# Kernel tuning notes

Hardware: AMD Instinct MI355X
Metric: run time of the kernel (lower is better)

Reference implementation:

```python
import jax, jax.numpy as jnp
import numpy as np

N_NODES = 50000
N_EDGES = 800000
D_IN = 128
D_HID = 128
GN_EPS = 1e-5
L2_EPS = 1e-12


def _gcn_conv(x, edge_index, W, b, num_nodes):
    """PyG GCNConv: symmetric normalization with self-loops; x [N, Fin]."""
    src, dst = edge_index[0], edge_index[1]
    loops = jnp.arange(num_nodes, dtype=src.dtype)
    src = jnp.concatenate([src, loops])
    dst = jnp.concatenate([dst, loops])
    ew = jnp.ones(src.shape[0], dtype=x.dtype)
    deg = jax.ops.segment_sum(ew, dst, num_segments=num_nodes)
    dinv = jnp.where(deg > 0, jax.lax.rsqrt(deg), 0.0)
    norm = dinv[src] * dinv[dst]                       # [E+N]
    xw = x @ W                                         # [N, Fout]
    msg = xw[src] * norm[:, None]                      # gather + scale
    out = jax.ops.segment_sum(msg, dst, num_segments=num_nodes)
    return out + b


def _message_norm(x, msg, scale):
    """PyG MessageNorm(learn_scale=True): x + scale * ||x|| * msg/||msg||."""
    msg_n = msg / jnp.maximum(jnp.linalg.norm(msg, axis=-1, keepdims=True), L2_EPS)
    x_norm = jnp.linalg.norm(x, axis=-1, keepdims=True)
    return x + scale * x_norm * msg_n


def _graph_norm(x, weight, bias, mean_scale):
    """PyG GraphNorm, single graph (batch all zeros)."""
    mean = jnp.mean(x, axis=0, keepdims=True)
    out = x - mean * mean_scale
    var = jnp.mean(out * out, axis=0, keepdims=True)
    return weight * out * jax.lax.rsqrt(var + GN_EPS) + bias


def _gelu(x):
    return jax.nn.gelu(x, approximate=False)


def setup_inputs() -> dict:
    key = jax.random.key(0)
    ks = jax.random.split(key, 4)
    X = jax.random.normal(ks[0], (D_IN, N_NODES), dtype=jnp.float32)
    edge_index = jax.random.randint(ks[1], (2, N_EDGES), 0, N_NODES, dtype=jnp.int64)
    W1 = jax.random.normal(ks[2], (D_IN, D_HID), dtype=jnp.float32) * (1.0 / np.sqrt(D_IN))
    b1 = jnp.zeros((D_HID,), dtype=jnp.float32)
    scale1 = jnp.ones((1,), dtype=jnp.float32)
    W2 = jax.random.normal(ks[3], (D_HID, D_IN), dtype=jnp.float32) * (1.0 / np.sqrt(D_HID))
    b2 = jnp.zeros((D_IN,), dtype=jnp.float32)
    scale2 = jnp.ones((1,), dtype=jnp.float32)
    gn_weight = jnp.ones((D_IN,), dtype=jnp.float32)
    gn_bias = jnp.zeros((D_IN,), dtype=jnp.float32)
    gn_mean_scale = jnp.ones((D_IN,), dtype=jnp.float32)
    return {"X": X, "edge_index": edge_index, "W1": W1, "b1": b1, "scale1": scale1,
            "W2": W2, "b2": b2, "scale2": scale2, "gn_weight": gn_weight,
            "gn_bias": gn_bias, "gn_mean_scale": gn_mean_scale}


def reference(X, edge_index, W1, b1, scale1, W2, b2, scale2,
              gn_weight, gn_bias, gn_mean_scale):
    x = X.T                                            # [N, D_IN]
    n = x.shape[0]
    # GCNChain 1
    f = _gelu(_message_norm(x, _gcn_conv(x, edge_index, W1, b1, n), scale1))
    # GCNChain 2
    f = _gelu(_message_norm(f, _gcn_conv(f, edge_index, W2, b2, n), scale2))
    # residual + GraphNorm + GELU
    return _gelu(_graph_norm(f + x, gn_weight, gn_bias, gn_mean_scale))
```

## Files before the change

kernel.cpp:

```cpp
#include <hip/hip_runtime.h>
#include <math.h>

#define D 128
#define CAP 64
#define NBUCK 98
#define BSZ   512
#define CAPB  10240
#define FSPLIT 4
#define FB (BSZ/FSPLIT)

typedef _Float16 h8 __attribute__((ext_vector_type(8)));
typedef float f4x __attribute__((ext_vector_type(4)));

__device__ __forceinline__ float gelu_f(float v){
    return 0.5f * v * (1.0f + erff(v * 0.70710678f));
}

__device__ __forceinline__ void unpack8(uint4 I, int* s){
    s[0] = (int)(I.x & 0xFFFFu); s[1] = (int)(I.x >> 16);
    s[2] = (int)(I.y & 0xFFFFu); s[3] = (int)(I.y >> 16);
    s[4] = (int)(I.z & 0xFFFFu); s[5] = (int)(I.z >> 16);
    s[6] = (int)(I.w & 0xFFFFu); s[7] = (int)(I.w >> 16);
}

__device__ __forceinline__ h8 gather_accum(const h8* __restrict__ y,
                                           const unsigned short* __restrict__ sp,
                                           int m, int lane, h8 a0){
    h8 z = {0,0,0,0,0,0,0,0};
    h8 a1 = z, a2 = z, a3 = z;
    int j = 0;
    for (; j + 16 <= m; j += 16){
        const uint4* spv = (const uint4*)(sp + j);
        uint4 I0 = spv[0], I1 = spv[1];
        int s[16];
        unpack8(I0, s); unpack8(I1, s + 8);
        h8 v[16];
        #pragma unroll
        for (int i = 0; i < 16; i++) v[i] = y[(size_t)s[i]*16 + lane];
        #pragma unroll
        for (int i = 0; i < 16; i += 4){
            a0 += v[i]; a1 += v[i+1]; a2 += v[i+2]; a3 += v[i+3];
        }
    }
    for (; j + 8 <= m; j += 8){
        const uint4* spv = (const uint4*)(sp + j);
        uint4 I0 = spv[0];
        int s[8];
        unpack8(I0, s);
        h8 v[8];
        #pragma unroll
        for (int i = 0; i < 8; i++) v[i] = y[(size_t)s[i]*16 + lane];
        #pragma unroll
        for (int i = 0; i < 8; i += 4){
            a0 += v[i]; a1 += v[i+1]; a2 += v[i+2]; a3 += v[i+3];
        }
    }
    for (; j + 4 <= m; j += 4){
        const uint2* spv = (const uint2*)(sp + j);
        uint2 I = spv[0];
        int s0 = (int)(I.x & 0xFFFFu), s1 = (int)(I.x >> 16);
        int s2 = (int)(I.y & 0xFFFFu), s3 = (int)(I.y >> 16);
        h8 v0 = y[(size_t)s0*16 + lane];
        h8 v1 = y[(size_t)s1*16 + lane];
        h8 v2 = y[(size_t)s2*16 + lane];
        h8 v3 = y[(size_t)s3*16 + lane];
        a0 += v0; a1 += v1; a2 += v2; a3 += v3;
    }
    for (; j < m; j++) a1 += y[(size_t)sp[j]*16 + lane];
    return (a0 + a1) + (a2 + a3);
}

__global__ void k_init(float* colsum, float* colsq, int* gcur,
                       const float* __restrict__ W1, const float* __restrict__ W2,
                       _Float16* __restrict__ wz1, _Float16* __restrict__ wz2){
    int i = blockIdx.x*blockDim.x + threadIdx.x;
    if (i < D){ colsum[i] = 0.f; colsq[i] = 0.f; }
    if (i < NBUCK) gcur[i] = 0;
    if (i < 32768){
        const float* W = (i < 16384) ? W1 : W2;
        _Float16* wz   = (i < 16384) ? wz1 : wz2;
        int u = i & 16383;
        int jj = u & 7, l = (u>>3)&63, fi = u>>9;
        int kb = fi>>3, j = fi&7;
        int k = kb*32 + (l>>4)*8 + jj;
        int c = j*16 + (l&15);
        wz[u] = (_Float16)W[k*D + c];
    }
}

__global__ __launch_bounds__(256)
void k_part(const int* __restrict__ ei, int* __restrict__ gcur,
            unsigned int* __restrict__ ebin, int E){
    __shared__ int bcnt[NBUCK], bbase[NBUCK], bcur[NBUCK];
    int t = threadIdx.x;
    int chunk = (E + gridDim.x - 1) / gridDim.x;
    int e0 = blockIdx.x*chunk, e1 = min(e0 + chunk, E);
    if (t < NBUCK){ bcnt[t] = 0; bcur[t] = 0; }
    __syncthreads();
    int sl[13], dl[13];
    #pragma unroll
    for (int k = 0; k < 13; k++){
        int e = e0 + t + k*256;
        sl[k] = -1;
        if (e < e1){
            sl[k] = __builtin_nontemporal_load(&ei[e]);
            dl[k] = __builtin_nontemporal_load(&ei[E + e]);
            atomicAdd(&bcnt[dl[k] >> 9], 1);
        }
    }
    __syncthreads();
    if (t < NBUCK) bbase[t] = atomicAdd(&gcur[t], bcnt[t]);
    __syncthreads();
    #pragma unroll
    for (int k = 0; k < 13; k++){
        if (sl[k] >= 0){
            int d = dl[k], b = d >> 9;
            int p = atomicAdd(&bcur[b], 1);
            int idx = bbase[b] + p;
            if (idx < CAPB)
                ebin[(size_t)b*CAPB + idx] = ((unsigned)(d & (BSZ-1)) << 16) | (unsigned)sl[k];
        }
    }
}

__global__ __launch_bounds__(256)
void k_fill2(const unsigned int* __restrict__ ebin, const int* __restrict__ gcur,
             int* __restrict__ cnt, unsigned short* __restrict__ csrc, int N){
    __shared__ unsigned short slab[FB*CAP];
    __shared__ int lcnt[FB];
    int bb = blockIdx.x, b = bb >> 2, part = bb & 3;
    int t = threadIdx.x;
    for (int i = t; i < FB; i += 256) lcnt[i] = 0;
    __syncthreads();
    int cntb = gcur[b]; if (cntb > CAPB) cntb = CAPB;
    const unsigned int* bp = ebin + (size_t)b*CAPB;
    for (int e = t; e < cntb; e += 256){
        unsigned pk = __builtin_nontemporal_load(&bp[e]);
        int dl = pk >> 16;
        if ((dl >> 7) == part){
            int dsub = dl & (FB-1);
            int p = atomicAdd(&lcnt[dsub], 1);
            if (p < CAP) slab[dsub*CAP + p] = (unsigned short)(pk & 0xFFFF);
        }
    }
    __syncthreads();
    int base = b*BSZ + part*FB;
    int nvalid = N - base; if (nvalid > FB) nvalid = FB; if (nvalid < 0) nvalid = 0;
    uint4* dst = (uint4*)&csrc[(size_t)base*CAP];
    const uint4* src = (const uint4*)slab;
    for (int i = t; i < nvalid*8; i += 256) dst[i] = src[i];
    for (int i = t; i < nvalid; i += 256) cnt[base + i] = lcnt[i];
}

__launch_bounds__(256)
__global__ void k_gemm_mfma(const float* __restrict__ in, const h8* __restrict__ wz,
                            const int* __restrict__ cnt, _Float16* __restrict__ outh,
                            h8* __restrict__ xt16, int N){
    __shared__ _Float16 a_lds[8192];
    int t = threadIdx.x;
    int n0 = blockIdx.x * 64;

    #pragma unroll
    for (int i = 0; i < 32; i++){
        int idx = i*256 + t;
        int k = idx >> 6, nn = idx & 63;
        int n = n0 + nn;
        float v = (n < N) ? in[(size_t)k*N + n] : 0.f;
        int kb = k>>5, ks = k&31;
        int lane = (ks>>3)*16 + (nn&15);
        int w = nn>>4;
        a_lds[((kb*4 + w)*64 + lane)*8 + (ks&7)] = (_Float16)v;
    }
    __syncthreads();

    int w = t>>6, l = t&63;
    f4x acc[8];
    #pragma unroll
    for (int j = 0; j < 8; j++) acc[j] = (f4x){0.f, 0.f, 0.f, 0.f};
    #pragma unroll
    for (int kb = 0; kb < 4; kb++){
        h8 a = *(const h8*)&a_lds[((kb*4 + w)*64 + l)*8];
        #pragma unroll
        for (int j = 0; j < 8; j++){
            h8 b = wz[(kb*8 + j)*64 + l];
            acc[j] = __builtin_amdgcn_mfma_f32_16x16x32_f16(a, b, acc[j], 0, 0, 0);
        }
    }

    int quad = l>>4, m = l&15;
    #pragma unroll
    for (int r = 0; r < 4; r++){
        int node = n0 + w*16 + quad*4 + r;
        if (node < N){
            float dv = rsqrtf((float)(cnt[node] + 1));
            #pragma unroll
            for (int j = 0; j < 8; j++)
                outh[(size_t)node*D + j*16 + m] = (_Float16)(acc[j][r] * dv);
        }
    }

    {
        int node = t>>2, kb = t&3;
        int n = n0 + node;
        if (n < N){
            #pragma unroll
            for (int q = 0; q < 4; q++){
                h8 v = *(const h8*)&a_lds[((kb*4 + (node>>4))*64 + q*16 + (node&15))*8];
                xt16[(size_t)n*16 + kb*4 + q] = v;
            }
        }
    }
}

__launch_bounds__(256, 4)
__global__ void k_gath1(const h8* __restrict__ y, const h8* __restrict__ resid,
                        const int* __restrict__ cnt,
                        const unsigned short* __restrict__ csrc,
                        const float* __restrict__ bias, const float* __restrict__ scale,
                        const h8* __restrict__ wz,
                        h8* __restrict__ f1out, _Float16* __restrict__ y2out, int N){
    __shared__ _Float16 a_lds[16*17*8];
    int t = threadIdx.x;
    int n0 = blockIdx.x * 16;
    int g = t >> 4, lane = t & 15;
    int n = n0 + g;
    bool valid = (n < N);

    h8 a0 = {0,0,0,0,0,0,0,0};
    int m = 0; float dv = 1.f;
    if (valid){
        int mraw = cnt[n];
        dv = rsqrtf((float)(mraw + 1));
        m = (mraw < CAP) ? mraw : CAP;
        a0 = y[(size_t)n*16 + lane];
    }
    const unsigned short* sp = csrc + (size_t)n*CAP;
    h8 ah = gather_accum(y, sp, m, lane, a0);

    const float4* bp = (const float4*)&bias[lane*8];
    float4 b0 = bp[0], b1v = bp[1];
    float c[8], r[8];
    float nc = 0.f, nr = 0.f;
    h8 rv = {0,0,0,0,0,0,0,0};
    if (valid) rv = resid[(size_t)n*16 + lane];
    #pragma unroll
    for (int i = 0; i < 8; i++){
        float bb = (i < 4) ? (&b0.x)[i] : (&b1v.x)[i-4];
        c[i] = bb + dv * (float)ah[i];
        nc += c[i]*c[i];
        r[i] = (float)rv[i];
        nr += r[i]*r[i];
    }
    #pragma unroll
    for (int mm = 8; mm > 0; mm >>= 1){
        nc += __shfl_xor(nc, mm, 64);
        nr += __shfl_xor(nr, mm, 64);
    }
    float scl = scale[0] * sqrtf(nr) / fmaxf(sqrtf(nc), 1e-12f);
    h8 o = {0,0,0,0,0,0,0,0};
    if (valid){
        #pragma unroll
        for (int i = 0; i < 8; i++) o[i] = (_Float16)gelu_f(r[i] + scl*c[i]);
        f1out[(size_t)n*16 + lane] = o;
    }
    *(h8*)&a_lds[(g*17 + lane)*8] = o;
    __syncthreads();

    int w = t >> 6, l = t & 63;
    f4x acc0 = {0.f,0.f,0.f,0.f}, acc1 = acc0;
    #pragma unroll
    for (int kb = 0; kb < 4; kb++){
        h8 a = *(const h8*)&a_lds[((l&15)*17 + kb*4 + (l>>4))*8];
        h8 bb0 = wz[(kb*8 + w*2+0)*64 + l];
        h8 bb1 = wz[(kb*8 + w*2+1)*64 + l];
        acc0 = __builtin_amdgcn_mfma_f32_16x16x32_f16(a, bb0, acc0, 0, 0, 0);
        acc1 = __builtin_amdgcn_mfma_f32_16x16x32_f16(a, bb1, acc1, 0, 0, 0);
    }
    int quad = l >> 4, mc = l & 15;
    #pragma unroll
    for (int r2 = 0; r2 < 4; r2++){
        int node = n0 + quad*4 + r2;
        if (node < N){
            float dvn = rsqrtf((float)(cnt[node] + 1));
            y2out[(size_t)node*D + (w*2+0)*16 + mc] = (_Float16)(acc0[r2] * dvn);
            y2out[(size_t)node*D + (w*2+1)*16 + mc] = (_Float16)(acc1[r2] * dvn);
        }
    }
}

__launch_bounds__(256, 4)
__global__ void k_gather2(const h8* __restrict__ y, const h8* __restrict__ resid,
                          const h8* __restrict__ xorig,
                          const int* __restrict__ cnt,
                          const unsigned short* __restrict__ csrc,
                          const float* __restrict__ bias, const float* __restrict__ scale,
                          h8* __restrict__ out16, int N){
    int n = blockIdx.x*16 + (threadIdx.x >> 4);
    if (n >= N) return;
    int lane = threadIdx.x & 15;
    h8 a0 = y[(size_t)n*16 + lane];
    int mraw = cnt[n];
    float dv = rsqrtf((float)(mraw + 1));
    int m = (mraw < CAP) ? mraw : CAP;
    const unsigned short* sp = csrc + (size_t)n*CAP;
    h8 ah = gather_accum(y, sp, m, lane, a0);

    const float4* bp = (const float4*)&bias[lane*8];
    float4 b0 = bp[0], b1v = bp[1];
    float c[8], r[8];
    float nc = 0.f, nr = 0.f;
    h8 rv = resid[(size_t)n*16 + lane];
    #pragma unroll
    for (int i = 0; i < 8; i++){
        float bb = (i < 4) ? (&b0.x)[i] : (&b1v.x)[i-4];
        c[i] = bb + dv * (float)ah[i];
        nc += c[i]*c[i];
        r[i] = (float)rv[i];
        nr += r[i]*r[i];
    }
    #pragma unroll
    for (int mm = 8; mm > 0; mm >>= 1){
        nc += __shfl_xor(nc, mm, 64);
        nr += __shfl_xor(nr, mm, 64);
    }
    float scl = scale[0] * sqrtf(nr) / fmaxf(sqrtf(nc), 1e-12f);
    h8 xv = xorig[(size_t)n*16 + lane];
    h8 o;
    #pragma unroll
    for (int i = 0; i < 8; i++)
        o[i] = (_Float16)(gelu_f(r[i] + scl*c[i]) + (float)xv[i]);
    out16[(size_t)n*16 + lane] = o;
}

__global__ void k_stats(const _Float16* __restrict__ h, float* colsum, float* colsq, int N){
    __shared__ float ls[256], ls2[256];
    int t = threadIdx.x;
    int f = t & 127, half = t >> 7;
    float s = 0.f, s2 = 0.f;
    for (int n = blockIdx.x*2 + half; n < N; n += gridDim.x*2){
        float v = (float)h[(size_t)n*D + f]; s += v; s2 += v*v;
    }
    ls[t] = s; ls2[t] = s2;
    __syncthreads();
    if (t < 128){
        s  = ls[t]  + ls[t+128];
        s2 = ls2[t] + ls2[t+128];
        atomicAdd(&colsum[f], s);
        atomicAdd(&colsq[f], s2);
    }
}

__global__ void k_final(const h8* __restrict__ h16,
                        const float* __restrict__ colsum, const float* __restrict__ colsq,
                        const float* __restrict__ gw, const float* __restrict__ gb,
                        const float* __restrict__ ms,
                        float* __restrict__ outp, int N){
    __shared__ float cf[D], sh[D];
    int t = threadIdx.x;
    if (t < D){
        float invN = 1.0f / (float)N;
        float mean = colsum[t] * invN;
        float c = mean * ms[t];
        float var = colsq[t]*invN - 2.f*c*mean + c*c;
        float a = gw[t] * rsqrtf(var + 1e-5f);
        cf[t] = a;
        sh[t] = gb[t] - c*a;
    }
    __syncthreads();
    int i = blockIdx.x*blockDim.x + t;
    if (i < N*16){
        int n = i >> 4, lane = i & 15;
        h8 v = h16[i];
        int f = lane*8;
        float4 o0, o1;
        o0.x = gelu_f((float)v[0]*cf[f+0] + sh[f+0]);
        o0.y = gelu_f((float)v[1]*cf[f+1] + sh[f+1]);
        o0.z = gelu_f((float)v[2]*cf[f+2] + sh[f+2]);
        o0.w = gelu_f((float)v[3]*cf[f+3] + sh[f+3]);
        o1.x = gelu_f((float)v[4]*cf[f+4] + sh[f+4]);
        o1.y = gelu_f((float)v[5]*cf[f+5] + sh[f+5]);
        o1.z = gelu_f((float)v[6]*cf[f+6] + sh[f+6]);
        o1.w = gelu_f((float)v[7]*cf[f+7] + sh[f+7]);
        *(float4*)&outp[(size_t)n*D + f]     = o0;
        *(float4*)&outp[(size_t)n*D + f + 4] = o1;
    }
}

extern "C" void kernel_launch(void* const* d_in, const int* in_sizes, int n_in,
                              void* d_out, int out_size, void* d_ws, size_t ws_size,
                              hipStream_t stream){
    const float* X   = (const float*)d_in[0];
    const int*   ei  = (const int*)  d_in[1];
    const float* W1  = (const float*)d_in[2];
    const float* b1  = (const float*)d_in[3];
    const float* s1  = (const float*)d_in[4];
    const float* W2  = (const float*)d_in[5];
    const float* b2  = (const float*)d_in[6];
    const float* s2  = (const float*)d_in[7];
    const float* gw  = (const float*)d_in[8];
    const float* gb  = (const float*)d_in[9];
    const float* gms = (const float*)d_in[10];
    int N = in_sizes[0] / D;
    int E = in_sizes[1] / 2;
    float* out = (float*)d_out;

    char* ws = (char*)d_ws;
    size_t o = 0;
    auto alloc = [&](size_t bytes)->void*{
        o = (o + 255) & ~(size_t)255;
        void* p = ws + o; o += bytes; return p;
    };
    int*            cnt    = (int*)           alloc((size_t)N * sizeof(int));
    unsigned short* csrc   = (unsigned short*)alloc((size_t)N * CAP * sizeof(unsigned short));
    unsigned int*   ebin   = (unsigned int*)  alloc((size_t)NBUCK * CAPB * sizeof(unsigned int));
    int*            gcur   = (int*)           alloc(NBUCK * sizeof(int));
    float*          colsum = (float*)         alloc(D * sizeof(float));
    float*          colsq  = (float*)         alloc(D * sizeof(float));
    _Float16*       wz1    = (_Float16*)      alloc(16384 * sizeof(_Float16));
    _Float16*       wz2    = (_Float16*)      alloc(16384 * sizeof(_Float16));
    _Float16*       A      = (_Float16*)      alloc((size_t)N * D * sizeof(_Float16));
    _Float16*       A2     = (_Float16*)      alloc((size_t)N * D * sizeof(_Float16));
    h8*             XT16   = (h8*)            alloc((size_t)N * D * sizeof(_Float16));
    h8*             F1     = (h8*)            alloc((size_t)N * D * sizeof(_Float16));
    h8*             B16    = (h8*)            alloc((size_t)N * D * sizeof(_Float16));

    k_init<<<128, 256, 0, stream>>>(colsum, colsq, gcur, W1, W2, wz1, wz2);
    k_part<<<256, 256, 0, stream>>>(ei, gcur, ebin, E);
    k_fill2<<<NBUCK*FSPLIT, 256, 0, stream>>>(ebin, gcur, cnt, csrc, N);

    k_gemm_mfma<<<(N+63)/64, 256, 0, stream>>>(X, (const h8*)wz1, cnt, A, XT16, N);
    k_gath1<<<(N+15)/16, 256, 0, stream>>>((const h8*)A, XT16, cnt, csrc, b1, s1,
                                           (const h8*)wz2, F1, A2, N);
    k_gather2<<<(N+15)/16, 256, 0, stream>>>((const h8*)A2, F1, XT16,
                                             cnt, csrc, b2, s2, B16, N);
    k_stats<<<256, 256, 0, stream>>>((const _Float16*)B16, colsum, colsq, N);
    k_final<<<(N*16+255)/256, 256, 0, stream>>>(B16, colsum, colsq, gw, gb, gms, out, N);
}
```

Before: 264.1 us.

## Pipeline neighbor gathers through LDS with async global_load_lds double buffering

Replaces the register-based neighbor gather loop in both gather kernels with a software pipeline. Each wave stages its neighbor indices in LDS and issues global_load_lds transfers of neighbor feature rows into a two-slot LDS ring, using explicit vmcnt/lgkmcnt waits so loads stay in flight while earlier slots are summed. Per-node loop trip counts are taken as the maximum across the wave, with per-node masking of the adds. This adds LDS usage (which may reduce occupancy), wasted loads for nodes with fewer neighbors, and depends on hand-placed waitcnt and sched_barrier ordering being correct.

Measured after the change: 273.8 us. +3.7%, slower.

```diff
diff --git a/kernel.cpp b/kernel.cpp
--- a/kernel.cpp
+++ b/kernel.cpp
@@ -16,58 +16,76 @@
     return 0.5f * v * (1.0f + erff(v * 0.70710678f));
 }
 
-__device__ __forceinline__ void unpack8(uint4 I, int* s){
-    s[0] = (int)(I.x & 0xFFFFu); s[1] = (int)(I.x >> 16);
-    s[2] = (int)(I.y & 0xFFFFu); s[3] = (int)(I.y >> 16);
-    s[4] = (int)(I.z & 0xFFFFu); s[5] = (int)(I.z >> 16);
-    s[6] = (int)(I.w & 0xFFFFu); s[7] = (int)(I.w >> 16);
-}
-
-__device__ __forceinline__ h8 gather_accum(const h8* __restrict__ y,
-                                           const unsigned short* __restrict__ sp,
-                                           int m, int lane, h8 a0){
+__device__ __forceinline__ void gload_lds16(const void* g, void* l){
+    typedef __attribute__((address_space(1))) const unsigned int g_u32;
+    typedef __attribute__((address_space(3))) unsigned int l_u32;
+    __builtin_amdgcn_global_load_lds((g_u32*)g, (l_u32*)l, 16, 0, 0);
+}
+
+__device__ __forceinline__ h8 gather_pipe(const char* __restrict__ yb,
+                                          uint4* ringw,
+                                          const unsigned short* idxg,
+                                          int m, int l, int Nm1, h8 A0){
     h8 z = {0,0,0,0,0,0,0,0};
-    h8 a1 = z, a2 = z, a3 = z;
-    int j = 0;
-    for (; j + 16 <= m; j += 16){
-        const uint4* spv = (const uint4*)(sp + j);
-        uint4 I0 = spv[0], I1 = spv[1];
-        int s[16];
-        unpack8(I0, s); unpack8(I1, s + 8);
-        h8 v[16];
-        #pragma unroll
-        for (int i = 0; i < 16; i++) v[i] = y[(size_t)s[i]*16 + lane];
-        #pragma unroll
-        for (int i = 0; i < 16; i += 4){
-            a0 += v[i]; a1 += v[i+1]; a2 += v[i+2]; a3 += v[i+3];
-        }
-    }
-    for (; j + 8 <= m; j += 8){
-        const uint4* spv = (const uint4*)(sp + j);
-        uint4 I0 = spv[0];
-        int s[8];
-        unpack8(I0, s);
-        h8 v[8];
-        #pragma unroll
-        for (int i = 0; i < 8; i++) v[i] = y[(size_t)s[i]*16 + lane];
-        #pragma unroll
-        for (int i = 0; i < 8; i += 4){
-            a0 += v[i]; a1 += v[i+1]; a2 += v[i+2]; a3 += v[i+3];
-        }
-    }
-    for (; j + 4 <= m; j += 4){
-        const uint2* spv = (const uint2*)(sp + j);
-        uint2 I = spv[0];
-        int s0 = (int)(I.x & 0xFFFFu), s1 = (int)(I.x >> 16);
-        int s2 = (int)(I.y & 0xFFFFu), s3 = (int)(I.y >> 16);
-        h8 v0 = y[(size_t)s0*16 + lane];
-        h8 v1 = y[(size_t)s1*16 + lane];
-        h8 v2 = y[(size_t)s2*16 + lane];
-        h8 v3 = y[(size_t)s3*16 + lane];
-        a0 += v0; a1 += v1; a2 += v2; a3 += v3;
-    }
-    for (; j < m; j++) a1 += y[(size_t)sp[j]*16 + lane];
-    return (a0 + a1) + (a2 + a3);
+    h8 A1 = z, A2 = z, A3 = z;
+    int t16 = __shfl_xor(m, 16);
+    int M = (m > t16) ? m : t16;
+    int t32 = __shfl_xor(M, 32);
+    M = (M > t32) ? M : t32;
+    int nq = (M + 3) >> 2;
+
+    auto issueq = [&](int q){
+        uint2 iv = *(const uint2*)(idxg + q*4);
+        uint4* sb = ringw + (q & 1) * 256;
+        unsigned u0 = iv.x & 0xFFFFu, u1 = iv.x >> 16;
+        unsigned u2 = iv.y & 0xFFFFu, u3 = iv.y >> 16;
+        u0 = (u0 > (unsigned)Nm1) ? (unsigned)Nm1 : u0;
+        u1 = (u1 > (unsigned)Nm1) ? (unsigned)Nm1 : u1;
+        u2 = (u2 > (unsigned)Nm1) ? (unsigned)Nm1 : u2;
+        u3 = (u3 > (unsigned)Nm1) ? (unsigned)Nm1 : u3;
+        gload_lds16(yb + ((size_t)u0 << 8), sb);
+        gload_lds16(yb + ((size_t)u1 << 8), sb + 64);
+        gload_lds16(yb + ((size_t)u2 << 8), sb + 128);
+        gload_lds16(yb + ((size_t)u3 << 8), sb + 192);
+    };
+    auto consq = [&](int q){
+        const uint4* sb = ringw + (q & 1) * 256 + l;
+        int j0 = q << 2;
+        h8 v0 = *(const h8*)(sb);
+        h8 v1 = *(const h8*)(sb + 64);
+        h8 v2 = *(const h8*)(sb + 128);
+        h8 v3 = *(const h8*)(sb + 192);
+        if (j0     < m) A0 += v0;
+        if (j0 + 1 < m) A1 += v1;
+        if (j0 + 2 < m) A2 += v2;
+        if (j0 + 3 < m) A3 += v3;
+    };
+
+    asm volatile("s_waitcnt vmcnt(0)" ::: "memory");
+    __builtin_amdgcn_sched_barrier(0);
+    if (nq >= 2){
+        issueq(0); issueq(1);
+        for (int q = 0; q < nq - 2; q++){
+            asm volatile("s_waitcnt vmcnt(4)" ::: "memory");
+            __builtin_amdgcn_sched_barrier(0);
+            consq(q);
+            asm volatile("s_waitcnt lgkmcnt(0)" ::: "memory");
+            __builtin_amdgcn_sched_barrier(0);
+            issueq(q + 2);
+        }
+        asm volatile("s_waitcnt vmcnt(4)" ::: "memory");
+        __builtin_amdgcn_sched_barrier(0);
+        consq(nq - 2);
+        asm volatile("s_waitcnt vmcnt(0)" ::: "memory");
+        __builtin_amdgcn_sched_barrier(0);
+        consq(nq - 1);
+    } else if (nq == 1){
+        issueq(0);
+        asm volatile("s_waitcnt vmcnt(0)" ::: "memory");
+        __builtin_amdgcn_sched_barrier(0);
+        consq(0);
+    }
+    return (A0 + A1) + (A2 + A3);
 }
 
 __global__ void k_init(float* colsum, float* colsq, int* gcur,
@@ -219,30 +237,38 @@
                         const float* __restrict__ bias, const float* __restrict__ scale,
                         const h8* __restrict__ wz,
                         h8* __restrict__ f1out, _Float16* __restrict__ y2out, int N){
+    __shared__ uint4 ring4[4][512];
+    __shared__ __align__(16) unsigned short idxb[16][64];
     __shared__ _Float16 a_lds[16*17*8];
     int t = threadIdx.x;
     int n0 = blockIdx.x * 16;
-    int g = t >> 4, lane = t & 15;
+    int g = t >> 4, f = t & 15;
+    int w = t >> 6, l = t & 63;
     int n = n0 + g;
     bool valid = (n < N);
 
-    h8 a0 = {0,0,0,0,0,0,0,0};
-    int m = 0; float dv = 1.f;
+    uint2 iw; iw.x = 0u; iw.y = 0u;
+    if (valid) iw = ((const uint2*)(csrc + (size_t)n*CAP))[f];
+    *(uint2*)&idxb[g][f*4] = iw;
+
+    int mraw = valid ? cnt[n] : 0;
+    float dv = rsqrtf((float)(mraw + 1));
+    int m = (mraw < CAP) ? mraw : CAP;
+    h8 z = {0,0,0,0,0,0,0,0};
+    h8 A0 = z, rv = z;
     if (valid){
-        int mraw = cnt[n];
-        dv = rsqrtf((float)(mraw + 1));
-        m = (mraw < CAP) ? mraw : CAP;
-        a0 = y[(size_t)n*16 + lane];
-    }
-    const unsigned short* sp = csrc + (size_t)n*CAP;
-    h8 ah = gather_accum(y, sp, m, lane, a0);
-
-    const float4* bp = (const float4*)&bias[lane*8];
+        A0 = y[(size_t)n*16 + f];
+        rv = resid[(size_t)n*16 + f];
+    }
+    const float4* bp = (const float4*)&bias[f*8];
     float4 b0 = bp[0], b1v = bp[1];
+    float sc0 = scale[0];
+
+    const char* yb = (const char*)y + (f << 4);
+    h8 ah = gather_pipe(yb, &ring4[w][0], &idxb[g][0], m, l, N - 1, A0);
+
     float c[8], r[8];
     float nc = 0.f, nr = 0.f;
-    h8 rv = {0,0,0,0,0,0,0,0};
-    if (valid) rv = resid[(size_t)n*16 + lane];
     #pragma unroll
     for (int i = 0; i < 8; i++){
         float bb = (i < 4) ? (&b0.x)[i] : (&b1v.x)[i-4];
@@ -256,17 +282,16 @@
         nc += __shfl_xor(nc, mm, 64);
         nr += __shfl_xor(nr, mm, 64);
     }
-    float scl = scale[0] * sqrtf(nr) / fmaxf(sqrtf(nc), 1e-12f);
-    h8 o = {0,0,0,0,0,0,0,0};
+    float scl = sc0 * sqrtf(nr) / fmaxf(sqrtf(nc), 1e-12f);
+    h8 o = z;
     if (valid){
         #pragma unroll
         for (int i = 0; i < 8; i++) o[i] = (_Float16)gelu_f(r[i] + scl*c[i]);
-        f1out[(size_t)n*16 + lane] = o;
-    }
-    *(h8*)&a_lds[(g*17 + lane)*8] = o;
-    __syncthreads();
-
-    int w = t >> 6, l = t & 63;
+        f1out[(size_t)n*16 + f] = o;
+    }
+    *(h8*)&a_lds[(g*17 + f)*8] = o;
+    __syncthreads();
+
     f4x acc0 = {0.f,0.f,0.f,0.f}, acc1 = acc0;
     #pragma unroll
     for (int kb = 0; kb < 4; kb++){
@@ -295,21 +320,38 @@
                           const unsigned short* __restrict__ csrc,
                           const float* __restrict__ bias, const float* __restrict__ scale,
                           h8* __restrict__ out16, int N){
-    int n = blockIdx.x*16 + (threadIdx.x >> 4);
-    if (n >= N) return;
-    int lane = threadIdx.x & 15;
-    h8 a0 = y[(size_t)n*16 + lane];
-    int mraw = cnt[n];
+    __shared__ uint4 ring4[4][512];
+    __shared__ __align__(16) unsigned short idxb[16][64];
+    int t = threadIdx.x;
+    int n0 = blockIdx.x * 16;
+    int g = t >> 4, f = t & 15;
+    int w = t >> 6, l = t & 63;
+    int n = n0 + g;
+    bool valid = (n < N);
+
+    uint2 iw; iw.x = 0u; iw.y = 0u;
+    if (valid) iw = ((const uint2*)(csrc + (size_t)n*CAP))[f];
+    *(uint2*)&idxb[g][f*4] = iw;
+
+    int mraw = valid ? cnt[n] : 0;
     float dv = rsqrtf((float)(mraw + 1));
     int m = (mraw < CAP) ? mraw : CAP;
-    const unsigned short* sp = csrc + (size_t)n*CAP;
-    h8 ah = gather_accum(y, sp, m, lane, a0);
-
-    const float4* bp = (const float4*)&bias[lane*8];
+    h8 z = {0,0,0,0,0,0,0,0};
+    h8 A0 = z, rv = z, xv = z;
+    if (valid){
+        A0 = y[(size_t)n*16 + f];
+        rv = resid[(size_t)n*16 + f];
+        xv = xorig[(size_t)n*16 + f];
+    }
+    const float4* bp = (const float4*)&bias[f*8];
     float4 b0 = bp[0], b1v = bp[1];
+    float sc0 = scale[0];
+
+    const char* yb = (const char*)y + (f << 4);
+    h8 ah = gather_pipe(yb, &ring4[w][0], &idxb[g][0], m, l, N - 1, A0);
+
     float c[8], r[8];
     float nc = 0.f, nr = 0.f;
-    h8 rv = resid[(size_t)n*16 + lane];
     #pragma unroll
     for (int i = 0; i < 8; i++){
         float bb = (i < 4) ? (&b0.x)[i] : (&b1v.x)[i-4];
@@ -323,13 +365,14 @@
         nc += __shfl_xor(nc, mm, 64);
         nr += __shfl_xor(nr, mm, 64);
     }
-    float scl = scale[0] * sqrtf(nr) / fmaxf(sqrtf(nc), 1e-12f);
-    h8 xv = xorig[(size_t)n*16 + lane];
-    h8 o;
-    #pragma unroll
-    for (int i = 0; i < 8; i++)
-        o[i] = (_Float16)(gelu_f(r[i] + scl*c[i]) + (float)xv[i]);
-    out16[(size_t)n*16 + lane] = o;
+    float scl = sc0 * sqrtf(nr) / fmaxf(sqrtf(nc), 1e-12f);
+    if (valid){
+        h8 o;
+        #pragma unroll
+        for (int i = 0; i < 8; i++)
+            o[i] = (_Float16)(gelu_f(r[i] + scl*c[i]) + (float)xv[i]);
+        out16[(size_t)n*16 + f] = o;
+    }
 }
 
 __global__ void k_stats(const _Float16* __restrict__ h, float* colsum, float* colsq, int N){
```
